# Kernel optimization log

Hardware: AMD Instinct MI355X
Metric: run time of the kernel (lower is better)

The kernel has to match this reference:

```python
import jax, jax.numpy as jnp
import numpy as np

TOPK = 8            # args.topk
SWAP_RATIO = 0.3    # args.swap_ratio
NUM_SPECIAL = 999   # first non-special wordpiece id in bert-base-uncased


def setup_inputs() -> dict:
    key = jax.random.key(0)
    k0, k1, k2, k3, k4, k5 = jax.random.split(key, 6)
    B, S, V, D = 4, 512, 30522, 768
    return {
        "delta_grad": jax.random.normal(k0, (B, S, D), jnp.float32),
        "src_embeds": jax.random.normal(k1, (B, S, D), jnp.float32),
        "embedding_matrix": jax.random.normal(k2, (V, D), jnp.float32),
        "src_tokens": jax.random.randint(k3, (B, S), 0, V),
        "pred_lm": jax.random.normal(k4, (B, S, V), jnp.float32),
        "attention_mask": jnp.ones((B, S), jnp.int32),
        "rand_u": jax.random.uniform(k5, (B, S), jnp.float32),
    }


def reference(delta_grad, src_embeds, embedding_matrix, src_tokens, pred_lm, attention_mask, rand_u):
    B, S, D = delta_grad.shape
    V = embedding_matrix.shape[0]
    neg_inf = jnp.float32(-np.inf)

    # dir_dot_grad = -(prev_dot - new_dot) = new_dot - prev_dot
    new_dot = jnp.einsum('bsd,vd->bsv', delta_grad, embedding_matrix)   # [B,S,V]
    prev_dot = jnp.einsum('bsd,bsd->bs', delta_grad, src_embeds)        # [B,S]
    dir_dot_grad = new_dot - prev_dot[..., None]

    # pairwise euclidean distance between src_embeds and vocab embeddings
    src_sq = jnp.sum(src_embeds * src_embeds, axis=-1)                  # [B,S]
    vocab_sq = jnp.sum(embedding_matrix * embedding_matrix, axis=-1)    # [V]
    dot = jnp.einsum('bsd,vd->bsv', src_embeds, embedding_matrix)       # [B,S,V]
    sq_norm = src_sq[..., None] + vocab_sq[None, None, :] - 2.0 * dot
    dir_norm = jnp.sqrt(jax.nn.relu(sq_norm) + 1e-20)

    dir_dot_grad = dir_dot_grad / dir_norm

    # LM top-k allowed-token mask (scatter of 0 into a -inf mask in torch)
    _, topk_idx = jax.lax.top_k(pred_lm, TOPK)                          # [B,S,K]
    topk_idx = topk_idx * attention_mask[..., None].astype(topk_idx.dtype)
    bi = jnp.arange(B)[:, None, None]
    si = jnp.arange(S)[None, :, None]
    allowed = jnp.zeros((B, S, V), bool).at[bi, si, topk_idx].set(True)

    filtered = jnp.where(allowed, dir_dot_grad, neg_inf)
    # special tokens [:999] -> -inf (overrides any topk scatter there)
    filtered = jnp.where(jnp.arange(V)[None, None, :] < NUM_SPECIAL, neg_inf, filtered)
    # forbid keeping the original token
    filtered = jnp.where(jnp.arange(V)[None, None, :] == src_tokens[..., None], neg_inf, filtered)

    adv_flip = jnp.argmax(filtered, axis=2)                             # [B,S]

    # swap mask: non-special positions, Bernoulli(swap_ratio)
    no_special = src_tokens >= NUM_SPECIAL
    swap = rand_u > (1.0 - SWAP_RATIO)
    mask_idx = (no_special & swap).astype(src_tokens.dtype)

    adv_tokens = src_tokens * (1 - mask_idx) + adv_flip.astype(src_tokens.dtype) * mask_idx
    return adv_tokens
```

## Files before the change

kernel.cpp:

```cpp
#include <hip/hip_runtime.h>
#include <math.h>

constexpr int TOPK = 8;
constexpr int NUM_SPECIAL = 999;
constexpr int V = 30522;
constexpr int D = 768;
constexpr int BLOCK = 256;
constexpr int NF4 = 7630;
constexpr int NK4 = 30;
constexpr int CAP = 512;
constexpr int HOTCAP = 64;

__device__ __forceinline__ unsigned long long fkey(float v, unsigned int idx) {
    unsigned int u = __float_as_uint(v);
    u = ((int)u < 0) ? ~u : (u | 0x80000000u);
    return ((unsigned long long)u << 32) | (unsigned long long)(~idx);
}

__device__ __forceinline__ void cmpx(float& a, float& b) {
    float m = fmaxf(a, b), n = fminf(a, b); a = m; b = n;
}

__device__ __forceinline__ void sort8_desc(float (&c)[8]) {
    cmpx(c[0],c[1]); cmpx(c[2],c[3]); cmpx(c[4],c[5]); cmpx(c[6],c[7]);
    cmpx(c[0],c[2]); cmpx(c[1],c[3]); cmpx(c[1],c[2]);
    cmpx(c[4],c[6]); cmpx(c[5],c[7]); cmpx(c[5],c[6]);
    cmpx(c[0],c[4]); cmpx(c[1],c[5]); cmpx(c[2],c[6]); cmpx(c[3],c[7]);
    cmpx(c[2],c[4]); cmpx(c[3],c[5]);
    cmpx(c[1],c[2]); cmpx(c[3],c[4]); cmpx(c[5],c[6]);
}

__device__ __forceinline__ void merge_top8(float (&R)[8], const float (&C)[8]) {
    float m[8];
    #pragma unroll
    for (int j = 0; j < 8; ++j) m[j] = fmaxf(R[j], C[7 - j]);
    cmpx(m[0],m[4]); cmpx(m[1],m[5]); cmpx(m[2],m[6]); cmpx(m[3],m[7]);
    cmpx(m[0],m[2]); cmpx(m[1],m[3]); cmpx(m[4],m[6]); cmpx(m[5],m[7]);
    cmpx(m[0],m[1]); cmpx(m[2],m[3]); cmpx(m[4],m[5]); cmpx(m[6],m[7]);
    #pragma unroll
    for (int j = 0; j < 8; ++j) R[j] = m[j];
}

__device__ __forceinline__ void net8(float (&L)[TOPK], float t) {
    #pragma unroll
    for (int j = 0; j < TOPK; ++j) {
        float m = fmaxf(L[j], t); t = fminf(L[j], t); L[j] = m;
    }
}

__device__ __forceinline__ void wave_extract8(float (&cur)[TOPK], int lane,
                                              float* dst) {
    #pragma unroll
    for (int r = 0; r < TOPK; ++r) {
        float m = cur[0];
        int ml = lane;
        #pragma unroll
        for (int off = 1; off < 64; off <<= 1) {
            float om = __shfl_xor(m, off, 64);
            int   ol = __shfl_xor(ml, off, 64);
            if (om > m || (om == m && ol < ml)) { m = om; ml = ol; }
        }
        if (lane == ml) {
            #pragma unroll
            for (int j = 0; j < TOPK - 1; ++j) cur[j] = cur[j + 1];
            cur[TOPK - 1] = -INFINITY;
        }
        if (lane == 0) dst[r] = m;
    }
}

__global__ __launch_bounds__(BLOCK, 8) void dvat_kernel(
    const float* __restrict__ delta_grad,
    const float* __restrict__ src_embeds,
    const float* __restrict__ emb,
    const int*   __restrict__ src_tokens,
    const float* __restrict__ pred_lm,
    const int*   __restrict__ attn,
    const float* __restrict__ rand_u,
    int* __restrict__ out)
{
    const int pos = blockIdx.x;
    const int tid = threadIdx.x;
    const int lane = tid & 63;
    const int wave = tid >> 6;

    __shared__ float  sm32[32];
    __shared__ float  s_g8;
    __shared__ int    s_hot[HOTCAP];
    __shared__ int    s_nhot;
    __shared__ int    s_ncand;
    __shared__ unsigned long long sh_cand64[CAP];
    __shared__ int    s_cand[TOPK];
    __shared__ double s_scores[TOPK];
    __shared__ double s_pd[4], s_ssq[4];
    __shared__ float  shf[2 * D];

    if (tid == 0) { s_nhot = 0; s_ncand = 0; }

    {
        const float* dg = delta_grad + (size_t)pos * D;
        const float* se = src_embeds + (size_t)pos * D;
        double pd = 0.0, ssq = 0.0;
        if (tid < D / 4) {
            float4 g = ((const float4*)dg)[tid];
            float4 e = ((const float4*)se)[tid];
            ((float4*)shf)[tid] = g;
            ((float4*)(shf + D))[tid] = e;
            pd  = (double)g.x * e.x + (double)g.y * e.y
                + (double)g.z * e.z + (double)g.w * e.w;
            ssq = (double)e.x * e.x + (double)e.y * e.y
                + (double)e.z * e.z + (double)e.w * e.w;
        }
        #pragma unroll
        for (int off = 32; off; off >>= 1) {
            pd  += __shfl_down(pd, off, 64);
            ssq += __shfl_down(ssq, off, 64);
        }
        if (lane == 0) { s_pd[wave] = pd; s_ssq[wave] = ssq; }
    }

    const float* row = pred_lm + (size_t)pos * V;
    const int al = (pos & 1) ? 2 : 0;
    const float4* f4 = (const float4*)(row + al);

    float R[8];
    #pragma unroll
    for (int j = 0; j < 8; ++j) R[j] = -INFINITY;

    int ia = tid;
    for (int p = 0; p < 7; ++p, ia += 4 * BLOCK) {
        float4 a = f4[ia];
        float4 b = f4[ia + BLOCK];
        float4 c = f4[ia + 2 * BLOCK];
        float4 d = f4[ia + 3 * BLOCK];
        float ca[8] = {a.x, a.y, a.z, a.w, b.x, b.y, b.z, b.w};
        sort8_desc(ca); merge_top8(R, ca);
        float cb[8] = {c.x, c.y, c.z, c.w, d.x, d.y, d.z, d.w};
        sort8_desc(cb); merge_top8(R, cb);
    }
    {
        float4 a = f4[ia];
        float4 b = {-INFINITY, -INFINITY, -INFINITY, -INFINITY};
        if (ia + BLOCK < NF4) b = f4[ia + BLOCK];
        float ca[8] = {a.x, a.y, a.z, a.w, b.x, b.y, b.z, b.w};
        sort8_desc(ca); merge_top8(R, ca);
    }
    if (tid == 0) {
        if (al) { net8(R, row[0]);     net8(R, row[1]); }
        else    { net8(R, row[V - 2]); net8(R, row[V - 1]); }
    }
    const float tmax = R[0];

    wave_extract8(R, lane, &sm32[wave * 8]);
    __syncthreads();

    if (wave == 0) {
        float c = (lane < 32) ? sm32[lane] : -INFINITY;
        float m = -INFINITY;
        #pragma unroll
        for (int r = 0; r < TOPK; ++r) {
            m = c; int ml = lane;
            #pragma unroll
            for (int off = 1; off < 64; off <<= 1) {
                float om = __shfl_xor(m, off, 64);
                int   ol = __shfl_xor(ml, off, 64);
                if (om > m || (om == m && ol < ml)) { m = om; ml = ol; }
            }
            if (lane == ml) c = -INFINITY;
        }
        if (lane == 0) s_g8 = m;
    }
    __syncthreads();
    const float g8 = s_g8;

    if (tmax >= g8) {
        int p = atomicAdd(&s_nhot, 1);
        if (p < HOTCAP) s_hot[p] = tid;
    }
    if (tid == 0) {
        if (al) {
            if (row[0] >= g8) { int p = atomicAdd(&s_ncand, 1); if (p < CAP) sh_cand64[p] = fkey(row[0], 0u); }
            if (row[1] >= g8) { int p = atomicAdd(&s_ncand, 1); if (p < CAP) sh_cand64[p] = fkey(row[1], 1u); }
        } else {
            if (row[V-2] >= g8) { int p = atomicAdd(&s_ncand, 1); if (p < CAP) sh_cand64[p] = fkey(row[V-2], (unsigned)(V-2)); }
            if (row[V-1] >= g8) { int p = atomicAdd(&s_ncand, 1); if (p < CAP) sh_cand64[p] = fkey(row[V-1], (unsigned)(V-1)); }
        }
    }
    __syncthreads();

    if (s_nhot <= HOTCAP) {
        const int nhot = s_nhot;
        const int total = nhot * NK4;
        for (int w = tid; w < total; w += BLOCK) {
            const int h = w / NK4;
            const int k = w - h * NK4;
            const int i4 = s_hot[h] + (k << 8);
            if (i4 < NF4) {
                float4 f = f4[i4];
                const unsigned base = (unsigned)(al + 4 * i4);
                if (f.x >= g8) { int p = atomicAdd(&s_ncand, 1); if (p < CAP) sh_cand64[p] = fkey(f.x, base); }
                if (f.y >= g8) { int p = atomicAdd(&s_ncand, 1); if (p < CAP) sh_cand64[p] = fkey(f.y, base + 1); }
                if (f.z >= g8) { int p = atomicAdd(&s_ncand, 1); if (p < CAP) sh_cand64[p] = fkey(f.z, base + 2); }
                if (f.w >= g8) { int p = atomicAdd(&s_ncand, 1); if (p < CAP) sh_cand64[p] = fkey(f.w, base + 3); }
            }
        }
    } else {
        for (int i4 = tid; i4 < NF4; i4 += BLOCK) {
            float4 f = f4[i4];
            const unsigned base = (unsigned)(al + 4 * i4);
            if (f.x >= g8) { int p = atomicAdd(&s_ncand, 1); if (p < CAP) sh_cand64[p] = fkey(f.x, base); }
            if (f.y >= g8) { int p = atomicAdd(&s_ncand, 1); if (p < CAP) sh_cand64[p] = fkey(f.y, base + 1); }
            if (f.z >= g8) { int p = atomicAdd(&s_ncand, 1); if (p < CAP) sh_cand64[p] = fkey(f.z, base + 2); }
            if (f.w >= g8) { int p = atomicAdd(&s_ncand, 1); if (p < CAP) sh_cand64[p] = fkey(f.w, base + 3); }
        }
    }
    __syncthreads();
    const int ncand = min(s_ncand, CAP);

    for (int it = 0; it < TOPK; ++it) {
        if (tid < 64) {
            unsigned long long m = 0ull; int ms = 0;
            for (int j = tid; j < ncand; j += 64) {
                unsigned long long x = sh_cand64[j];
                if (x > m) { m = x; ms = j; }
            }
            #pragma unroll
            for (int off = 32; off; off >>= 1) {
                unsigned long long om = __shfl_down(m, off, 64);
                int os = __shfl_down(ms, off, 64);
                if (om > m) { m = om; ms = os; }
            }
            if (tid == 0) {
                s_cand[it] = (m == 0ull) ? 0 : (int)(~(unsigned int)m);
                sh_cand64[ms] = 0ull;
            }
        }
        __syncthreads();
    }

    if (tid == 0 && attn[pos] == 0) {
        #pragma unroll
        for (int k = 0; k < TOPK; ++k) s_cand[k] = 0;
    }
    __syncthreads();

    const double prev_dot = s_pd[0] + s_pd[1] + s_pd[2] + s_pd[3];
    const double src_sq   = s_ssq[0] + s_ssq[1] + s_ssq[2] + s_ssq[3];

    #pragma unroll
    for (int kk = 0; kk < 2; ++kk) {
        const int k = 2 * wave + kk;
        const int v = s_cand[k];
        const float* ev = emb + (size_t)v * D;
        double ddg = 0.0, dse = 0.0, dvv = 0.0;
        for (int ii = lane; ii < D; ii += 64) {
            double e = (double)ev[ii];
            ddg += e * (double)shf[ii];
            dse += e * (double)shf[D + ii];
            dvv += e * e;
        }
        #pragma unroll
        for (int off = 32; off; off >>= 1) {
            ddg += __shfl_down(ddg, off, 64);
            dse += __shfl_down(dse, off, 64);
            dvv += __shfl_down(dvv, off, 64);
        }
        if (lane == 0) {
            double sq = src_sq + dvv - 2.0 * dse;
            if (sq < 0.0) sq = 0.0;
            double dn = sqrt(sq + 1e-20);
            s_scores[k] = (ddg - prev_dot) / dn;
        }
    }
    __syncthreads();

    if (tid == 0) {
        const int src_tok = src_tokens[pos];
        int best = 0;
        double best_s = 0.0;
        bool found = false;
        #pragma unroll
        for (int k = 0; k < TOPK; ++k) {
            const int v = s_cand[k];
            if (v < NUM_SPECIAL || v == src_tok) continue;
            const double sc = s_scores[k];
            if (!found || sc > best_s || (sc == best_s && v < best)) {
                best = v; best_s = sc; found = true;
            }
        }
        const int adv_flip = found ? best : 0;
        const bool no_special = (src_tok >= NUM_SPECIAL);
        const bool swap = (rand_u[pos] > 0.7f);
        out[pos] = (no_special && swap) ? adv_flip : src_tok;
    }
}

extern "C" void kernel_launch(void* const* d_in, const int* in_sizes, int n_in,
                              void* d_out, int out_size, void* d_ws, size_t ws_size,
                              hipStream_t stream) {
    const float* delta_grad = (const float*)d_in[0];
    const float* src_embeds = (const float*)d_in[1];
    const float* emb        = (const float*)d_in[2];
    const int*   src_tokens = (const int*)d_in[3];
    const float* pred_lm    = (const float*)d_in[4];
    const int*   attn       = (const int*)d_in[5];
    const float* randu      = (const float*)d_in[6];
    int* out = (int*)d_out;

    const int BS = in_sizes[3];
    dvat_kernel<<<BS, BLOCK, 0, stream>>>(delta_grad, src_embeds, emb,
                                          src_tokens, pred_lm, attn, randu, out);
}
```

Baseline: 421.4 us.

## Split per-row top-k across four slice blocks with register-resident values and merge kernel

The top-k scan over pred_lm is moved into a separate kernel where each row is split into four slices, each handled by its own block. Each block keeps its slice values in registers (float2 loads), so candidate collection needs no second global read. Per-slice top-8 keys go to workspace, and a second kernel merges the 32 keys per row and computes the embedding scores. This raises parallelism from 2048 to 8192 blocks and removes the rescan of hot columns, at the cost of an extra launch and a workspace round trip.

```diff
diff --git a/kernel.cpp b/kernel.cpp
--- a/kernel.cpp
+++ b/kernel.cpp
@@ -6,10 +6,10 @@
 constexpr int V = 30522;
 constexpr int D = 768;
 constexpr int BLOCK = 256;
-constexpr int NF4 = 7630;
-constexpr int NK4 = 30;
-constexpr int CAP = 512;
-constexpr int HOTCAP = 64;
+constexpr int V2 = V / 2;
+constexpr int NSLICE = 4;
+constexpr int NL = 15;
+constexpr int CAP = 256;
 
 __device__ __forceinline__ unsigned long long fkey(float v, unsigned int idx) {
     unsigned int u = __float_as_uint(v);
@@ -41,13 +41,6 @@
     for (int j = 0; j < 8; ++j) R[j] = m[j];
 }
 
-__device__ __forceinline__ void net8(float (&L)[TOPK], float t) {
-    #pragma unroll
-    for (int j = 0; j < TOPK; ++j) {
-        float m = fmaxf(L[j], t); t = fminf(L[j], t); L[j] = m;
-    }
-}
-
 __device__ __forceinline__ void wave_extract8(float (&cur)[TOPK], int lane,
                                               float* dst) {
     #pragma unroll
@@ -69,37 +62,146 @@
     }
 }
 
-__global__ __launch_bounds__(BLOCK, 8) void dvat_kernel(
+__global__ __launch_bounds__(BLOCK) void topk_slice_kernel(
+    const float* __restrict__ pred_lm,
+    unsigned long long* __restrict__ ws_keys)
+{
+    const int row = blockIdx.x >> 2;
+    const int s   = blockIdx.x & 3;
+    const int tid = threadIdx.x;
+    const int lane = tid & 63;
+    const int wave = tid >> 6;
+
+    const int f2start = (s == 0) ? 0 : (3816 + 3815 * (s - 1));
+    const int cnt     = (s == 0) ? 3816 : 3815;
+
+    __shared__ float  sm32[32];
+    __shared__ float  s_g8;
+    __shared__ int    s_ncand;
+    __shared__ unsigned long long sh_cand[CAP];
+    __shared__ unsigned long long s_top[TOPK];
+
+    if (tid == 0) s_ncand = 0;
+
+    const float2* row2 = (const float2*)(pred_lm + (size_t)row * V) + f2start;
+    float2 arr[NL];
+    #pragma unroll
+    for (int k = 0; k < NL; ++k) {
+        const int idx = tid + (k << 8);
+        float2 v = make_float2(-INFINITY, -INFINITY);
+        if (idx < cnt) v = row2[idx];
+        arr[k] = v;
+    }
+
+    float R[8];
+    {
+        float c[8] = {arr[0].x, arr[0].y, arr[1].x, arr[1].y,
+                      arr[2].x, arr[2].y, arr[3].x, arr[3].y};
+        sort8_desc(c);
+        #pragma unroll
+        for (int j = 0; j < 8; ++j) R[j] = c[j];
+    }
+    {
+        float c[8] = {arr[4].x, arr[4].y, arr[5].x, arr[5].y,
+                      arr[6].x, arr[6].y, arr[7].x, arr[7].y};
+        sort8_desc(c); merge_top8(R, c);
+    }
+    {
+        float c[8] = {arr[8].x, arr[8].y, arr[9].x, arr[9].y,
+                      arr[10].x, arr[10].y, arr[11].x, arr[11].y};
+        sort8_desc(c); merge_top8(R, c);
+    }
+    {
+        float c[8] = {arr[12].x, arr[12].y, arr[13].x, arr[13].y,
+                      arr[14].x, arr[14].y, -INFINITY, -INFINITY};
+        sort8_desc(c); merge_top8(R, c);
+    }
+    const float tmax = R[0];
+
+    wave_extract8(R, lane, &sm32[wave * 8]);
+    __syncthreads();
+    if (wave == 0) {
+        float c = (lane < 32) ? sm32[lane] : -INFINITY;
+        float m = -INFINITY;
+        #pragma unroll
+        for (int r = 0; r < TOPK; ++r) {
+            m = c; int ml = lane;
+            #pragma unroll
+            for (int off = 1; off < 64; off <<= 1) {
+                float om = __shfl_xor(m, off, 64);
+                int   ol = __shfl_xor(ml, off, 64);
+                if (om > m || (om == m && ol < ml)) { m = om; ml = ol; }
+            }
+            if (lane == ml) c = -INFINITY;
+        }
+        if (lane == 0) s_g8 = m;
+    }
+    __syncthreads();
+    const float g8 = s_g8;
+
+    if (tmax >= g8) {
+        #pragma unroll
+        for (int k = 0; k < NL; ++k) {
+            const int idx = tid + (k << 8);
+            if (idx < cnt) {
+                const unsigned gbase = (unsigned)(2 * (f2start + idx));
+                if (arr[k].x >= g8) {
+                    int p = atomicAdd(&s_ncand, 1);
+                    if (p < CAP) sh_cand[p] = fkey(arr[k].x, gbase);
+                }
+                if (arr[k].y >= g8) {
+                    int p = atomicAdd(&s_ncand, 1);
+                    if (p < CAP) sh_cand[p] = fkey(arr[k].y, gbase + 1);
+                }
+            }
+        }
+    }
+    __syncthreads();
+    const int ncand = min(s_ncand, CAP);
+
+    if (wave == 0) {
+        for (int it = 0; it < TOPK; ++it) {
+            unsigned long long m = 0ull; int ms = 0;
+            for (int j = lane; j < ncand; j += 64) {
+                unsigned long long x = sh_cand[j];
+                if (x > m) { m = x; ms = j; }
+            }
+            #pragma unroll
+            for (int off = 1; off < 64; off <<= 1) {
+                unsigned long long om = __shfl_xor(m, off, 64);
+                int os = __shfl_xor(ms, off, 64);
+                if (om > m) { m = om; ms = os; }
+            }
+            if (lane == 0) { s_top[it] = m; sh_cand[ms] = 0ull; }
+        }
+        if (lane < TOPK)
+            ws_keys[((size_t)row * NSLICE + s) * TOPK + lane] = s_top[lane];
+    }
+}
+
+__global__ __launch_bounds__(BLOCK) void score_epilogue_kernel(
     const float* __restrict__ delta_grad,
     const float* __restrict__ src_embeds,
     const float* __restrict__ emb,
     const int*   __restrict__ src_tokens,
-    const float* __restrict__ pred_lm,
+    const unsigned long long* __restrict__ ws_keys,
     const int*   __restrict__ attn,
     const float* __restrict__ rand_u,
     int* __restrict__ out)
 {
-    const int pos = blockIdx.x;
+    const int row = blockIdx.x;
     const int tid = threadIdx.x;
     const int lane = tid & 63;
     const int wave = tid >> 6;
 
-    __shared__ float  sm32[32];
-    __shared__ float  s_g8;
-    __shared__ int    s_hot[HOTCAP];
-    __shared__ int    s_nhot;
-    __shared__ int    s_ncand;
-    __shared__ unsigned long long sh_cand64[CAP];
     __shared__ int    s_cand[TOPK];
     __shared__ double s_scores[TOPK];
     __shared__ double s_pd[4], s_ssq[4];
     __shared__ float  shf[2 * D];
 
-    if (tid == 0) { s_nhot = 0; s_ncand = 0; }
-
-    {
-        const float* dg = delta_grad + (size_t)pos * D;
-        const float* se = src_embeds + (size_t)pos * D;
+    {
+        const float* dg = delta_grad + (size_t)row * D;
+        const float* se = src_embeds + (size_t)row * D;
         double pd = 0.0, ssq = 0.0;
         if (tid < D / 4) {
             float4 g = ((const float4*)dg)[tid];
@@ -119,126 +221,25 @@
         if (lane == 0) { s_pd[wave] = pd; s_ssq[wave] = ssq; }
     }
 
-    const float* row = pred_lm + (size_t)pos * V;
-    const int al = (pos & 1) ? 2 : 0;
-    const float4* f4 = (const float4*)(row + al);
-
-    float R[8];
-    #pragma unroll
-    for (int j = 0; j < 8; ++j) R[j] = -INFINITY;
-
-    int ia = tid;
-    for (int p = 0; p < 7; ++p, ia += 4 * BLOCK) {
-        float4 a = f4[ia];
-        float4 b = f4[ia + BLOCK];
-        float4 c = f4[ia + 2 * BLOCK];
-        float4 d = f4[ia + 3 * BLOCK];
-        float ca[8] = {a.x, a.y, a.z, a.w, b.x, b.y, b.z, b.w};
-        sort8_desc(ca); merge_top8(R, ca);
-        float cb[8] = {c.x, c.y, c.z, c.w, d.x, d.y, d.z, d.w};
-        sort8_desc(cb); merge_top8(R, cb);
-    }
-    {
-        float4 a = f4[ia];
-        float4 b = {-INFINITY, -INFINITY, -INFINITY, -INFINITY};
-        if (ia + BLOCK < NF4) b = f4[ia + BLOCK];
-        float ca[8] = {a.x, a.y, a.z, a.w, b.x, b.y, b.z, b.w};
-        sort8_desc(ca); merge_top8(R, ca);
-    }
-    if (tid == 0) {
-        if (al) { net8(R, row[0]);     net8(R, row[1]); }
-        else    { net8(R, row[V - 2]); net8(R, row[V - 1]); }
-    }
-    const float tmax = R[0];
-
-    wave_extract8(R, lane, &sm32[wave * 8]);
-    __syncthreads();
-
     if (wave == 0) {
-        float c = (lane < 32) ? sm32[lane] : -INFINITY;
-        float m = -INFINITY;
+        unsigned long long c = (lane < NSLICE * TOPK)
+                             ? ws_keys[(size_t)row * (NSLICE * TOPK) + lane] : 0ull;
         #pragma unroll
         for (int r = 0; r < TOPK; ++r) {
-            m = c; int ml = lane;
+            unsigned long long m = c; int ml = lane;
             #pragma unroll
             for (int off = 1; off < 64; off <<= 1) {
-                float om = __shfl_xor(m, off, 64);
-                int   ol = __shfl_xor(ml, off, 64);
-                if (om > m || (om == m && ol < ml)) { m = om; ml = ol; }
-            }
-            if (lane == ml) c = -INFINITY;
-        }
-        if (lane == 0) s_g8 = m;
-    }
-    __syncthreads();
-    const float g8 = s_g8;
-
-    if (tmax >= g8) {
-        int p = atomicAdd(&s_nhot, 1);
-        if (p < HOTCAP) s_hot[p] = tid;
-    }
-    if (tid == 0) {
-        if (al) {
-            if (row[0] >= g8) { int p = atomicAdd(&s_ncand, 1); if (p < CAP) sh_cand64[p] = fkey(row[0], 0u); }
-            if (row[1] >= g8) { int p = atomicAdd(&s_ncand, 1); if (p < CAP) sh_cand64[p] = fkey(row[1], 1u); }
-        } else {
-            if (row[V-2] >= g8) { int p = atomicAdd(&s_ncand, 1); if (p < CAP) sh_cand64[p] = fkey(row[V-2], (unsigned)(V-2)); }
-            if (row[V-1] >= g8) { int p = atomicAdd(&s_ncand, 1); if (p < CAP) sh_cand64[p] = fkey(row[V-1], (unsigned)(V-1)); }
-        }
-    }
-    __syncthreads();
-
-    if (s_nhot <= HOTCAP) {
-        const int nhot = s_nhot;
-        const int total = nhot * NK4;
-        for (int w = tid; w < total; w += BLOCK) {
-            const int h = w / NK4;
-            const int k = w - h * NK4;
-            const int i4 = s_hot[h] + (k << 8);
-            if (i4 < NF4) {
-                float4 f = f4[i4];
-                const unsigned base = (unsigned)(al + 4 * i4);
-                if (f.x >= g8) { int p = atomicAdd(&s_ncand, 1); if (p < CAP) sh_cand64[p] = fkey(f.x, base); }
-                if (f.y >= g8) { int p = atomicAdd(&s_ncand, 1); if (p < CAP) sh_cand64[p] = fkey(f.y, base + 1); }
-                if (f.z >= g8) { int p = atomicAdd(&s_ncand, 1); if (p < CAP) sh_cand64[p] = fkey(f.z, base + 2); }
-                if (f.w >= g8) { int p = atomicAdd(&s_ncand, 1); if (p < CAP) sh_cand64[p] = fkey(f.w, base + 3); }
-            }
-        }
-    } else {
-        for (int i4 = tid; i4 < NF4; i4 += BLOCK) {
-            float4 f = f4[i4];
-            const unsigned base = (unsigned)(al + 4 * i4);
-            if (f.x >= g8) { int p = atomicAdd(&s_ncand, 1); if (p < CAP) sh_cand64[p] = fkey(f.x, base); }
-            if (f.y >= g8) { int p = atomicAdd(&s_ncand, 1); if (p < CAP) sh_cand64[p] = fkey(f.y, base + 1); }
-            if (f.z >= g8) { int p = atomicAdd(&s_ncand, 1); if (p < CAP) sh_cand64[p] = fkey(f.z, base + 2); }
-            if (f.w >= g8) { int p = atomicAdd(&s_ncand, 1); if (p < CAP) sh_cand64[p] = fkey(f.w, base + 3); }
-        }
-    }
-    __syncthreads();
-    const int ncand = min(s_ncand, CAP);
-
-    for (int it = 0; it < TOPK; ++it) {
-        if (tid < 64) {
-            unsigned long long m = 0ull; int ms = 0;
-            for (int j = tid; j < ncand; j += 64) {
-                unsigned long long x = sh_cand64[j];
-                if (x > m) { m = x; ms = j; }
-            }
-            #pragma unroll
-            for (int off = 32; off; off >>= 1) {
-                unsigned long long om = __shfl_down(m, off, 64);
-                int os = __shfl_down(ms, off, 64);
-                if (om > m) { m = om; ms = os; }
-            }
-            if (tid == 0) {
-                s_cand[it] = (m == 0ull) ? 0 : (int)(~(unsigned int)m);
-                sh_cand64[ms] = 0ull;
-            }
-        }
-        __syncthreads();
-    }
-
-    if (tid == 0 && attn[pos] == 0) {
+                unsigned long long om = __shfl_xor(m, off, 64);
+                int ol = __shfl_xor(ml, off, 64);
+                if (om > m) { m = om; ml = ol; }
+            }
+            if (lane == ml) c = 0ull;
+            if (lane == 0) s_cand[r] = (int)(~(unsigned int)m);
+        }
+    }
+    __syncthreads();
+
+    if (tid == 0 && attn[row] == 0) {
         #pragma unroll
         for (int k = 0; k < TOPK; ++k) s_cand[k] = 0;
     }
@@ -275,7 +276,7 @@
     __syncthreads();
 
     if (tid == 0) {
-        const int src_tok = src_tokens[pos];
+        const int src_tok = src_tokens[row];
         int best = 0;
         double best_s = 0.0;
         bool found = false;
@@ -290,8 +291,8 @@
         }
         const int adv_flip = found ? best : 0;
         const bool no_special = (src_tok >= NUM_SPECIAL);
-        const bool swap = (rand_u[pos] > 0.7f);
-        out[pos] = (no_special && swap) ? adv_flip : src_tok;
+        const bool swap = (rand_u[row] > 0.7f);
+        out[row] = (no_special && swap) ? adv_flip : src_tok;
     }
 }
 
@@ -308,6 +309,10 @@
     int* out = (int*)d_out;
 
     const int BS = in_sizes[3];
-    dvat_kernel<<<BS, BLOCK, 0, stream>>>(delta_grad, src_embeds, emb,
-                                          src_tokens, pred_lm, attn, randu, out);
-}
+    unsigned long long* ws_keys = (unsigned long long*)d_ws;
+
+    topk_slice_kernel<<<BS * NSLICE, BLOCK, 0, stream>>>(pred_lm, ws_keys);
+    score_epilogue_kernel<<<BS, BLOCK, 0, stream>>>(delta_grad, src_embeds, emb,
+                                                    src_tokens, ws_keys, attn,
+                                                    randu, out);
+}
```

After: 422.3 us. Within noise of the previous version (+0.2%).
